# Kernel optimization log

Measured on AMD Instinct MI355X. Metric: run time of the kernel, lower is better.

## Reference

```python
import jax, jax.numpy as jnp
import numpy as np

N_USER = 500_000
N_GROUP = 100_000
N_EDGE = 5_000_000
DIM = 64
NORM_2 = -1.0  # exponent for back-pass degree norm (module default)
ALPHA = 0.0    # residual mix coefficient (module default)


def setup_inputs() -> dict:
    key = jax.random.key(0)
    k1, k2, k3, k4 = jax.random.split(key, 4)
    h_user = jax.random.normal(k1, (N_USER, DIM), dtype=jnp.float32)
    h_group = jax.random.normal(k2, (N_GROUP, DIM), dtype=jnp.float32)
    edge_src = jax.random.randint(k3, (N_EDGE,), 0, N_USER, dtype=jnp.int64)
    edge_dst = jax.random.randint(k4, (N_EDGE,), 0, N_GROUP, dtype=jnp.int64)
    return {"h_user": h_user, "h_group": h_group,
            "edge_src": edge_src, "edge_dst": edge_dst}


def reference(h_user, h_group, edge_src, edge_dst):
    # Forward pass: copy_src -> sum aggregate onto dst, normalize by in-degree^-1.
    ones = jnp.ones((edge_src.shape[0],), dtype=h_user.dtype)
    deg_dst = jax.ops.segment_sum(ones, edge_dst, num_segments=N_GROUP)
    deg_dst = jnp.maximum(deg_dst, 1.0)  # clamp(min=1)
    rst = jax.ops.segment_sum(h_user[edge_src], edge_dst, num_segments=N_GROUP)
    if ALPHA != 0.0:
        rst = rst + ALPHA * h_group
    rst = rst * (1.0 / deg_dst)[:, None]  # [N_GROUP, DIM]
    # Back pass: aggregate rst back onto src via reversed edges, normalize by deg^norm_2.
    deg_src = jax.ops.segment_sum(ones, edge_src, num_segments=N_USER)
    deg_src = jnp.maximum(deg_src, 1.0)
    bsrc = jax.ops.segment_sum(rst[edge_dst], edge_src, num_segments=N_USER)
    bsrc = bsrc * jnp.power(deg_src, NORM_2)[:, None]  # [N_USER, DIM]
    return bsrc, rst
```

## Files before the change

### kernel.cpp

```cpp
#include <hip/hip_runtime.h>

#define N_USER  500000
#define N_GROUP 100000
#define N_EDGE  5000000
#define DIM     64

#define SCAN_BLOCK 256
#define SCAN_ELEMS 4096
#define PER_THREAD (SCAN_ELEMS / SCAN_BLOCK)

#define KD_SHIFT 7
#define KS_SHIFT 9
#define C_DST ((N_GROUP + (1 << KD_SHIFT) - 1) >> KD_SHIFT)
#define C_SRC ((N_USER  + (1 << KS_SHIFT) - 1) >> KS_SHIFT)
#define TILE_A 16384
#define CVT_BLOCKS 1024
#define CAP_D 7680
#define CAP_S 6272

typedef unsigned int uint32;

__device__ inline unsigned short f2bf(float x) {
    uint32 b = __float_as_uint(x);
    uint32 r = (b + 0x7FFFu + ((b >> 16) & 1u)) >> 16;
    return (unsigned short)r;
}
__device__ inline float ldt(const float* t, size_t i) { return t[i]; }
__device__ inline float ldt(const unsigned short* t, size_t i) {
    return __uint_as_float((uint32)t[i] << 16);
}

__global__ void prep_kernel(const int* __restrict__ src,
                            const int* __restrict__ dst,
                            int* __restrict__ ccd,
                            int* __restrict__ ccs,
                            const float* __restrict__ hin,
                            unsigned short* __restrict__ h16,
                            int gridA) {
    __shared__ int hd[C_DST], hs[C_SRC];
    int tid = threadIdx.x;
    if ((int)blockIdx.x < gridA) {
        long base = (long)blockIdx.x * TILE_A;
        for (int k = tid; k < C_DST; k += blockDim.x) hd[k] = 0;
        for (int k = tid; k < C_SRC; k += blockDim.x) hs[k] = 0;
        __syncthreads();
        for (int i = tid; i < TILE_A; i += blockDim.x) {
            long e = base + i;
            if (e >= N_EDGE) break;
            atomicAdd(&hd[dst[e] >> KD_SHIFT], 1);
            atomicAdd(&hs[src[e] >> KS_SHIFT], 1);
        }
        __syncthreads();
        for (int k = tid; k < C_DST; k += blockDim.x) if (hd[k]) atomicAdd(&ccd[k], hd[k]);
        for (int k = tid; k < C_SRC; k += blockDim.x) if (hs[k]) atomicAdd(&ccs[k], hs[k]);
    } else if (h16) {
        long n4 = (long)N_USER * DIM / 4;
        long stride = (long)CVT_BLOCKS * blockDim.x;
        for (long i = (long)(blockIdx.x - gridA) * blockDim.x + tid; i < n4; i += stride) {
            const float4 v = ((const float4*)hin)[i];
            ushort4 o;
            o.x = f2bf(v.x); o.y = f2bf(v.y); o.z = f2bf(v.z); o.w = f2bf(v.w);
            ((ushort4*)h16)[i] = o;
        }
    }
}

#define SS_PT 16
__global__ void small_scan(const int* __restrict__ cnt,
                           int* __restrict__ coff,
                           int* __restrict__ curs,
                           int n,
                           int* __restrict__ tail) {
    __shared__ int tsum[256];
    int tid = threadIdx.x;
    int local[SS_PT];
    int sum = 0;
    int base = tid * SS_PT;
#pragma unroll
    for (int i = 0; i < SS_PT; ++i) {
        int idx = base + i;
        int v = (idx < n) ? cnt[idx] : 0;
        local[i] = sum;
        sum += v;
    }
    tsum[tid] = sum;
    __syncthreads();
    for (int o = 1; o < 256; o <<= 1) {
        int t = (tid >= o) ? tsum[tid - o] : 0;
        __syncthreads();
        tsum[tid] += t;
        __syncthreads();
    }
    int texc = tsum[tid] - sum;
    int total = tsum[255];
#pragma unroll
    for (int i = 0; i < SS_PT; ++i) {
        int idx = base + i;
        if (idx < n) {
            int v = texc + local[i];
            coff[idx] = v;
            curs[idx * 16] = v;
        }
    }
    if (tid == 0) {
        coff[n] = total;
        if (tail) *tail = total;
    }
}

__global__ void scan1_kernel(const int* __restrict__ cnt,
                             int* __restrict__ off,
                             int* __restrict__ partial,
                             int n) {
    __shared__ int sh[SCAN_BLOCK];
    int tid = threadIdx.x;
    int tbase = blockIdx.x * SCAN_ELEMS + tid * PER_THREAD;
    int local[PER_THREAD];
    int sum = 0;
#pragma unroll
    for (int i = 0; i < PER_THREAD; ++i) {
        int idx = tbase + i;
        int v = (idx < n) ? cnt[idx] : 0;
        local[i] = sum;
        sum += v;
    }
    sh[tid] = sum;
    __syncthreads();
    for (int o = 1; o < SCAN_BLOCK; o <<= 1) {
        int t = (tid >= o) ? sh[tid - o] : 0;
        __syncthreads();
        sh[tid] += t;
        __syncthreads();
    }
    int texc = sh[tid] - sum;
    int blockTotal = sh[SCAN_BLOCK - 1];
#pragma unroll
    for (int i = 0; i < PER_THREAD; ++i) {
        int idx = tbase + i;
        if (idx < n) off[idx] = local[i] + texc;
    }
    if (tid == 0) partial[blockIdx.x] = blockTotal;
}

__global__ void scan2_kernel(int* __restrict__ partial, int nb,
                             int* __restrict__ off_end) {
    __shared__ int sh[SCAN_BLOCK];
    int tid = threadIdx.x;
    int v = (tid < nb) ? partial[tid] : 0;
    sh[tid] = v;
    __syncthreads();
    for (int o = 1; o < SCAN_BLOCK; o <<= 1) {
        int t = (tid >= o) ? sh[tid - o] : 0;
        __syncthreads();
        sh[tid] += t;
        __syncthreads();
    }
    if (tid < nb) partial[tid] = sh[tid] - v;
    if (tid == 0) *off_end = sh[SCAN_BLOCK - 1];
}

__global__ void scan3_kernel(int* __restrict__ off,
                             const int* __restrict__ partial, int n) {
    int base = blockIdx.x * SCAN_ELEMS;
    int add = partial[blockIdx.x];
    for (int i = threadIdx.x; i < SCAN_ELEMS; i += blockDim.x) {
        int idx = base + i;
        if (idx < n) off[idx] += add;
    }
}

__global__ void passA(const int* __restrict__ src,
                      const int* __restrict__ dst,
                      int* __restrict__ curs_cd,
                      int* __restrict__ curs_cs,
                      uint32* __restrict__ coarse_dst,
                      uint32* __restrict__ coarse_src) {
    __shared__ int hd[C_DST], bd[C_DST], hs[C_SRC], bs[C_SRC];
    int tid = threadIdx.x;
    long base = (long)blockIdx.x * TILE_A;

    for (int c = tid; c < C_DST; c += blockDim.x) hd[c] = 0;
    for (int c = tid; c < C_SRC; c += blockDim.x) hs[c] = 0;
    __syncthreads();

    for (int i = tid; i < TILE_A; i += blockDim.x) {
        long e = base + i;
        if (e >= N_EDGE) break;
        int g = dst[e], u = src[e];
        atomicAdd(&hd[g >> KD_SHIFT], 1);
        atomicAdd(&hs[u >> KS_SHIFT], 1);
    }
    __syncthreads();

    for (int c = tid; c < C_DST; c += blockDim.x) {
        int n = hd[c];
        bd[c] = n ? atomicAdd(&curs_cd[c * 16], n) : 0;
        hd[c] = 0;
    }
    for (int c = tid; c < C_SRC; c += blockDim.x) {
        int n = hs[c];
        bs[c] = n ? atomicAdd(&curs_cs[c * 16], n) : 0;
        hs[c] = 0;
    }
    __syncthreads();

    for (int i = tid; i < TILE_A; i += blockDim.x) {
        long e = base + i;
        if (e >= N_EDGE) break;
        int g = dst[e], u = src[e];
        int cd = g >> KD_SHIFT;
        int pd = atomicAdd(&hd[cd], 1);
        coarse_dst[(size_t)bd[cd] + pd] =
            ((uint32)(g & ((1 << KD_SHIFT) - 1)) << 20) | (uint32)u;
        int cs = u >> KS_SHIFT;
        int ps = atomicAdd(&hs[cs], 1);
        coarse_src[(size_t)bs[cs] + ps] =
            ((uint32)(u & ((1 << KS_SHIFT) - 1)) << 20) | (uint32)g;
    }
}

template <int SHIFT, int CAP, int U, bool NT, typename T>
__global__ __launch_bounds__(512) void sortgather(
    const uint32* __restrict__ coarse,
    const int* __restrict__ coarse_off,
    const T* __restrict__ table,
    float* __restrict__ out,
    unsigned short* __restrict__ out16,
    int n) {
    const int NK = 1 << SHIFT;
    __shared__ int vals[CAP];
    __shared__ int hist[NK];
    __shared__ int cur[NK];
    int tid = threadIdx.x;
    int c = blockIdx.x;
    int lo_g = c << SHIFT;
    int beg = coarse_off[c], end = coarse_off[c + 1];
    int cnt = end - beg;
    int stg = min(cnt, CAP);

    for (int k = tid; k < NK; k += 512) hist[k] = 0;
    __syncthreads();

    for (int i = tid; i < stg; i += 512) {
        uint32 kv = coarse[beg + i];
        atomicAdd(&hist[kv >> 20], 1);
    }
    __syncthreads();

    for (int o = 1; o < NK; o <<= 1) {
        int t = (tid < NK && tid >= o) ? hist[tid - o] : 0;
        __syncthreads();
        if (tid < NK) hist[tid] += t;
        __syncthreads();
    }
    if (tid < NK) cur[tid] = (tid == 0) ? 0 : hist[tid - 1];
    __syncthreads();

    for (int i = tid; i < stg; i += 512) {
        uint32 kv = coarse[beg + i];
        int p = atomicAdd(&cur[kv >> 20], 1);
        vals[p] = (int)(kv & 0xFFFFFu);
    }
    __syncthreads();

    int wv = tid >> 6, lane = tid & 63;
    for (int r = wv; r < NK; r += 8) {
        int row = lo_g + r;
        if (row >= n) break;
        int lo = (r == 0) ? 0 : hist[r - 1];
        int hi = hist[r];
        float a[U];
#pragma unroll
        for (int j = 0; j < U; ++j) a[j] = 0.0f;
        int e = lo;
        for (; e + U <= hi; e += U) {
#pragma unroll
            for (int j = 0; j < U; ++j) {
                int s = vals[e + j];
                a[j] += ldt(table, (size_t)s * DIM + lane);
            }
        }
        for (; e < hi; ++e) {
            int s = vals[e];
            a[0] += ldt(table, (size_t)s * DIM + lane);
        }
        int deg = hi - lo;
        if (stg < cnt) {
            for (int i = beg + stg; i < end; ++i) {
                uint32 kv = coarse[i];
                if ((int)(kv >> 20) == r) {
                    a[0] += ldt(table, (size_t)(kv & 0xFFFFFu) * DIM + lane);
                    ++deg;
                }
            }
        }
        float acc = 0.0f;
#pragma unroll
        for (int j = 0; j < U; ++j) acc += a[j];
        float rv = acc / fmaxf((float)deg, 1.0f);
        size_t oidx = (size_t)row * DIM + lane;
        if (NT) __builtin_nontemporal_store(rv, &out[oidx]);
        else out[oidx] = rv;
        if (out16) out16[oidx] = f2bf(rv);
    }
}

__global__ void hist_kernel(const int* __restrict__ src,
                            const int* __restrict__ dst,
                            int* __restrict__ cnt_src,
                            int* __restrict__ cnt_dst) {
    int e = blockIdx.x * blockDim.x + threadIdx.x;
    if (e < N_EDGE) {
        atomicAdd(&cnt_src[src[e]], 1);
        atomicAdd(&cnt_dst[dst[e]], 1);
    }
}

__global__ void fill_both(const int* __restrict__ src,
                          const int* __restrict__ dst,
                          const int* __restrict__ off_src,
                          const int* __restrict__ off_dst,
                          int* __restrict__ cur_src,
                          int* __restrict__ cur_dst,
                          int* __restrict__ bucket_src,
                          int* __restrict__ bucket_dst) {
    int e = blockIdx.x * blockDim.x + threadIdx.x;
    if (e < N_EDGE) {
        int u = src[e];
        int g = dst[e];
        int p = atomicAdd(&cur_src[u], 1);
        bucket_src[off_src[u] + p] = g;
        int q = atomicAdd(&cur_dst[g], 1);
        bucket_dst[off_dst[g] + q] = u;
    }
}

__global__ void fill_one(const int* __restrict__ key,
                         const int* __restrict__ val,
                         const int* __restrict__ off,
                         int* __restrict__ cur,
                         int* __restrict__ bucket) {
    int e = blockIdx.x * blockDim.x + threadIdx.x;
    if (e < N_EDGE) {
        int k = key[e];
        int p = atomicAdd(&cur[k], 1);
        bucket[off[k] + p] = val[e];
    }
}

__global__ void cvt_bf16(const float* __restrict__ in,
                         unsigned short* __restrict__ out, long n4) {
    long i = (long)blockIdx.x * blockDim.x + threadIdx.x;
    if (i >= n4) return;
    const float4 v = ((const float4*)in)[i];
    ushort4 o;
    o.x = f2bf(v.x); o.y = f2bf(v.y); o.z = f2bf(v.z); o.w = f2bf(v.w);
    ((ushort4*)out)[i] = o;
}

template <int NROW, bool NT, int U, typename T>
__global__ void gather_kernel(const int* __restrict__ off,
                              const int* __restrict__ bucket,
                              const T* __restrict__ table,
                              float* __restrict__ out,
                              unsigned short* __restrict__ out16) {
    int wid = (blockIdx.x * blockDim.x + threadIdx.x) >> 6;
    int lane = threadIdx.x & 63;
    if (wid >= NROW) return;
    int beg = off[wid], end = off[wid + 1];

    float a[U];
#pragma unroll
    for (int j = 0; j < U; ++j) a[j] = 0.0f;

    for (int b = beg; b < end; b += 64) {
        int navail = min(64, end - b);
        int sv = bucket[b + (lane < navail ? lane : 0)];
        int k = 0;
        for (; k + U <= navail; k += U) {
#pragma unroll
            for (int j = 0; j < U; ++j) {
                int s = __shfl(sv, k + j);
                a[j] += ldt(table, (size_t)s * DIM + lane);
            }
        }
        if (k < navail) {
#pragma unroll
            for (int j = 0; j < U; ++j) {
                int kk = k + j;
                int s = __shfl(sv, kk < navail ? kk : navail - 1);
                float w = (kk < navail) ? 1.0f : 0.0f;
                a[j] += w * ldt(table, (size_t)s * DIM + lane);
            }
        }
    }
    float acc = 0.0f;
#pragma unroll
    for (int j = 0; j < U; ++j) acc += a[j];
    float inv = 1.0f / fmaxf((float)(end - beg), 1.0f);
    float r = acc * inv;
    if (NT) {
        __builtin_nontemporal_store(r, &out[(size_t)wid * DIM + lane]);
    } else {
        out[(size_t)wid * DIM + lane] = r;
    }
    if (out16) out16[(size_t)wid * DIM + lane] = f2bf(r);
}

__global__ void deg_kernel(const int* __restrict__ src,
                           const int* __restrict__ dst,
                           float* __restrict__ deg_src,
                           float* __restrict__ deg_dst) {
    int e = blockIdx.x * blockDim.x + threadIdx.x;
    if (e < N_EDGE) {
        unsafeAtomicAdd(&deg_src[src[e]], 1.0f);
        unsafeAtomicAdd(&deg_dst[dst[e]], 1.0f);
    }
}

__global__ void scatter_fwd(const int* __restrict__ src,
                            const int* __restrict__ dst,
                            const float* __restrict__ h_user,
                            float* __restrict__ rst) {
    long idx = (long)blockIdx.x * blockDim.x + threadIdx.x;
    if (idx >= (long)N_EDGE * DIM) return;
    int e = (int)(idx >> 6), d = (int)(idx & 63);
    unsafeAtomicAdd(&rst[(long)dst[e] * DIM + d], h_user[(long)src[e] * DIM + d]);
}

__global__ void norm_kernel(float* __restrict__ x,
                            const float* __restrict__ deg, long total) {
    long idx = (long)blockIdx.x * blockDim.x + threadIdx.x;
    if (idx >= total) return;
    float dg = fmaxf(deg[idx >> 6], 1.0f);
    x[idx] *= (1.0f / dg);
}

__global__ void scatter_bwd(const int* __restrict__ src,
                            const int* __restrict__ dst,
                            const float* __restrict__ rst,
                            float* __restrict__ bsrc) {
    long idx = (long)blockIdx.x * blockDim.x + threadIdx.x;
    if (idx >= (long)N_EDGE * DIM) return;
    int e = (int)(idx >> 6), d = (int)(idx & 63);
    unsafeAtomicAdd(&bsrc[(long)src[e] * DIM + d], rst[(long)dst[e] * DIM + d]);
}

extern "C" void kernel_launch(void* const* d_in, const int* in_sizes, int n_in,
                              void* d_out, int out_size, void* d_ws, size_t ws_size,
                              hipStream_t stream) {
    const float* h_user   = (const float*)d_in[0];
    const int*   edge_src = (const int*)d_in[2];
    const int*   edge_dst = (const int*)d_in[3];

    float* bsrc = (float*)d_out;
    float* rst  = bsrc + (size_t)N_USER * DIM;

    const int BLK = 256;
    const int grid_e = (N_EDGE + BLK - 1) / BLK;

    int* ws      = (int*)d_ws;
    int* cnt_dst = ws;
    int* off_dst = cnt_dst + N_GROUP;
    int* cnt_src = off_dst + N_GROUP + 1;
    int* off_src = cnt_src + N_USER;
    int* cur_dst = off_src + N_USER + 1;
    int* cur_src = cur_dst + N_GROUP;
    int* partial = cur_src + N_USER;
    int* bucket_dst = partial + 256;
    int* bucket_src = bucket_dst + N_EDGE;
    unsigned short* r16 = (unsigned short*)(bucket_src + N_EDGE);
    unsigned short* h16 = r16 + (size_t)N_GROUP * DIM;
    size_t tail = ((size_t)((char*)(h16 + (size_t)N_USER * DIM) - (char*)d_ws) + 7) & ~(size_t)7;
    int* curs_cd = (int*)((char*)d_ws + tail);
    int* curs_cs = curs_cd + C_DST * 16;
    int* ccnt_d  = curs_cs + C_SRC * 16;
    int* ccnt_s  = ccnt_d + C_DST;
    int* coff_d  = ccnt_s + C_SRC;
    int* coff_s  = coff_d + C_DST + 1;
    size_t tail2 = ((size_t)((char*)(coff_s + C_SRC + 1) - (char*)d_ws) + 7) & ~(size_t)7;
    uint32* coarse_dst = (uint32*)((char*)d_ws + tail2);
    uint32* coarse_src = coarse_dst + N_EDGE;

    size_t need_csr1 = (size_t)((bucket_dst + N_EDGE) - ws) * sizeof(int);
    size_t need_csr2 = (size_t)((bucket_src + N_EDGE) - ws) * sizeof(int);
    size_t need_r16  = need_csr2 + (size_t)N_GROUP * DIM * 2;
    size_t need_full = need_r16 + (size_t)N_USER * DIM * 2;
    size_t need_ms   = (size_t)((char*)(coarse_src + N_EDGE) - (char*)d_ws);

    int nb_dst = (N_GROUP + SCAN_ELEMS - 1) / SCAN_ELEMS;
    int nb_src = (N_USER + SCAN_ELEMS - 1) / SCAN_ELEMS;

    if (ws_size >= need_ms) {
        bool use_h16 = (ws_size >= need_full);
        bool use_r16 = (ws_size >= need_r16);

        hipMemsetAsync(ccnt_d, 0, (size_t)(C_DST + C_SRC) * sizeof(int), stream);

        int gridA = (N_EDGE + TILE_A - 1) / TILE_A;
        int gridP = gridA + (use_h16 ? CVT_BLOCKS : 0);
        prep_kernel<<<gridP, BLK, 0, stream>>>(edge_src, edge_dst, ccnt_d, ccnt_s,
                                               h_user, use_h16 ? h16 : nullptr, gridA);

        small_scan<<<1, 256, 0, stream>>>(ccnt_d, coff_d, curs_cd, C_DST, nullptr);
        small_scan<<<1, 256, 0, stream>>>(ccnt_s, coff_s, curs_cs, C_SRC, nullptr);

        passA<<<gridA, BLK, 0, stream>>>(edge_src, edge_dst,
                                         curs_cd, curs_cs, coarse_dst, coarse_src);

        unsigned short* r16p = use_r16 ? r16 : (unsigned short*)nullptr;
        if (use_h16) {
            sortgather<KD_SHIFT, CAP_D, 8, false, unsigned short>
                <<<C_DST, 512, 0, stream>>>(coarse_dst, coff_d, h16, rst, r16p, N_GROUP);
        } else {
            sortgather<KD_SHIFT, CAP_D, 8, false, float>
                <<<C_DST, 512, 0, stream>>>(coarse_dst, coff_d, h_user, rst, r16p, N_GROUP);
        }
        if (use_r16) {
            sortgather<KS_SHIFT, CAP_S, 4, true, unsigned short>
                <<<C_SRC, 512, 0, stream>>>(coarse_src, coff_s, r16, bsrc, nullptr, N_USER);
        } else {
            sortgather<KS_SHIFT, CAP_S, 4, true, float>
                <<<C_SRC, 512, 0, stream>>>(coarse_src, coff_s, rst, bsrc, nullptr, N_USER);
        }
        return;
    }

    if (ws_size >= need_csr2) {
        bool use_h16 = (ws_size >= need_full);
        bool use_r16 = (ws_size >= need_r16);

        hipMemsetAsync(d_ws, 0, (size_t)(partial - ws) * sizeof(int), stream);

        if (use_h16) {
            long n4 = (long)N_USER * DIM / 4;
            cvt_bf16<<<(int)((n4 + BLK - 1) / BLK), BLK, 0, stream>>>(h_user, h16, n4);
        }

        hist_kernel<<<grid_e, BLK, 0, stream>>>(edge_src, edge_dst, cnt_src, cnt_dst);

        scan1_kernel<<<nb_dst, SCAN_BLOCK, 0, stream>>>(cnt_dst, off_dst, partial, N_GROUP);
        scan2_kernel<<<1, SCAN_BLOCK, 0, stream>>>(partial, nb_dst, off_dst + N_GROUP);
        scan3_kernel<<<nb_dst, SCAN_BLOCK, 0, stream>>>(off_dst, partial, N_GROUP);

        scan1_kernel<<<nb_src, SCAN_BLOCK, 0, stream>>>(cnt_src, off_src, partial, N_USER);
        scan2_kernel<<<1, SCAN_BLOCK, 0, stream>>>(partial, nb_src, off_src + N_USER);
        scan3_kernel<<<nb_src, SCAN_BLOCK, 0, stream>>>(off_src, partial, N_USER);

        fill_both<<<grid_e, BLK, 0, stream>>>(
            edge_src, edge_dst, off_src, off_dst,
            cur_src, cur_dst, bucket_src, bucket_dst);

        unsigned short* r16p = use_r16 ? r16 : (unsigned short*)nullptr;
        if (use_h16) {
            gather_kernel<N_GROUP, false, 8, unsigned short>
                <<<(N_GROUP * 64 + BLK - 1) / BLK, BLK, 0, stream>>>(
                    off_dst, bucket_dst, h16, rst, r16p);
        } else {
            gather_kernel<N_GROUP, false, 8, float>
                <<<(N_GROUP * 64 + BLK - 1) / BLK, BLK, 0, stream>>>(
                    off_dst, bucket_dst, h_user, rst, r16p);
        }
        if (use_r16) {
            gather_kernel<N_USER, true, 4, unsigned short>
                <<<(int)(((size_t)N_USER * 64 + BLK - 1) / BLK), BLK, 0, stream>>>(
                    off_src, bucket_src, r16, bsrc, nullptr);
        } else {
            gather_kernel<N_USER, true, 4, float>
                <<<(int)(((size_t)N_USER * 64 + BLK - 1) / BLK), BLK, 0, stream>>>(
                    off_src, bucket_src, rst, bsrc, nullptr);
        }
        return;
    }

    if (ws_size >= need_csr1) {
        hipMemsetAsync(d_ws, 0, (size_t)(partial - ws) * sizeof(int), stream);
        hist_kernel<<<grid_e, BLK, 0, stream>>>(edge_src, edge_dst, cnt_src, cnt_dst);

        scan1_kernel<<<nb_dst, SCAN_BLOCK, 0, stream>>>(cnt_dst, off_dst, partial, N_GROUP);
        scan2_kernel<<<1, SCAN_BLOCK, 0, stream>>>(partial, nb_dst, off_dst + N_GROUP);
        scan3_kernel<<<nb_dst, SCAN_BLOCK, 0, stream>>>(off_dst, partial, N_GROUP);

        scan1_kernel<<<nb_src, SCAN_BLOCK, 0, stream>>>(cnt_src, off_src, partial, N_USER);
        scan2_kernel<<<1, SCAN_BLOCK, 0, stream>>>(partial, nb_src, off_src + N_USER);
        scan3_kernel<<<nb_src, SCAN_BLOCK, 0, stream>>>(off_src, partial, N_USER);

        fill_one<<<grid_e, BLK, 0, stream>>>(edge_dst, edge_src, off_dst, cur_dst, bucket_dst);
        gather_kernel<N_GROUP, false, 8, float>
            <<<(N_GROUP * 64 + BLK - 1) / BLK, BLK, 0, stream>>>(
                off_dst, bucket_dst, h_user, rst, nullptr);

        fill_one<<<grid_e, BLK, 0, stream>>>(edge_src, edge_dst, off_src, cur_src, bucket_dst);
        gather_kernel<N_USER, true, 4, float>
            <<<(int)(((size_t)N_USER * 64 + BLK - 1) / BLK), BLK, 0, stream>>>(
                off_src, bucket_dst, rst, bsrc, nullptr);
        return;
    }

    float* deg_dst = (float*)d_ws;
    float* deg_src = deg_dst + N_GROUP;
    hipMemsetAsync(d_out, 0, (size_t)(N_USER + N_GROUP) * DIM * sizeof(float), stream);
    hipMemsetAsync(d_ws, 0, (size_t)(N_USER + N_GROUP) * sizeof(float), stream);

    deg_kernel<<<grid_e, BLK, 0, stream>>>(edge_src, edge_dst, deg_src, deg_dst);

    long total_ed = (long)N_EDGE * DIM;
    int grid_ed = (int)((total_ed + BLK - 1) / BLK);
    scatter_fwd<<<grid_ed, BLK, 0, stream>>>(edge_src, edge_dst, h_user, rst);
    long total_g = (long)N_GROUP * DIM;
    norm_kernel<<<(int)((total_g + BLK - 1) / BLK), BLK, 0, stream>>>(rst, deg_dst, total_g);
    scatter_bwd<<<grid_ed, BLK, 0, stream>>>(edge_src, edge_dst, rst, bsrc);
    long total_u = (long)N_USER * DIM;
    norm_kernel<<<(int)((total_u + BLK - 1) / BLK), BLK, 0, stream>>>(bsrc, deg_src, total_u);
}
```

Before: 597.9 us.

## Replace atomic bucket cursors with scanned per-block count matrix; split rst into halves

Each prep block now writes its per-bucket counts into a bucket-major count matrix, and a full three-stage scan over that matrix gives every block fixed write offsets. This removes the global atomics on bucket cursors and the second histogram pass in passA, and it also makes the scatter deterministic. The bf16 copy of rst is stored as two 32-column halves, and a new backward kernel gathers each half in its own pass, so every gathered row is 64 bytes. This is meant to improve cache hit rates on the random gathers. In exchange it adds six scan launches over the large matrices and reads the edge lists twice in the backward kernel.

```diff
diff --git a/kernel.cpp b/kernel.cpp
--- a/kernel.cpp
+++ b/kernel.cpp
@@ -14,9 +14,12 @@
 #define C_DST ((N_GROUP + (1 << KD_SHIFT) - 1) >> KD_SHIFT)
 #define C_SRC ((N_USER  + (1 << KS_SHIFT) - 1) >> KS_SHIFT)
 #define TILE_A 16384
+#define GRID_A ((N_EDGE + TILE_A - 1) / TILE_A)
 #define CVT_BLOCKS 1024
 #define CAP_D 7680
 #define CAP_S 6272
+#define MD_N (C_DST * GRID_A)
+#define MS_N (C_SRC * GRID_A)
 
 typedef unsigned int uint32;
 
@@ -32,15 +35,15 @@
 
 __global__ void prep_kernel(const int* __restrict__ src,
                             const int* __restrict__ dst,
-                            int* __restrict__ ccd,
-                            int* __restrict__ ccs,
+                            int* __restrict__ mat_d,
+                            int* __restrict__ mat_s,
                             const float* __restrict__ hin,
-                            unsigned short* __restrict__ h16,
-                            int gridA) {
+                            unsigned short* __restrict__ h16) {
     __shared__ int hd[C_DST], hs[C_SRC];
     int tid = threadIdx.x;
-    if ((int)blockIdx.x < gridA) {
-        long base = (long)blockIdx.x * TILE_A;
+    int b = blockIdx.x;
+    if (b < GRID_A) {
+        long base = (long)b * TILE_A;
         for (int k = tid; k < C_DST; k += blockDim.x) hd[k] = 0;
         for (int k = tid; k < C_SRC; k += blockDim.x) hs[k] = 0;
         __syncthreads();
@@ -51,60 +54,17 @@
             atomicAdd(&hs[src[e] >> KS_SHIFT], 1);
         }
         __syncthreads();
-        for (int k = tid; k < C_DST; k += blockDim.x) if (hd[k]) atomicAdd(&ccd[k], hd[k]);
-        for (int k = tid; k < C_SRC; k += blockDim.x) if (hs[k]) atomicAdd(&ccs[k], hs[k]);
+        for (int k = tid; k < C_DST; k += blockDim.x) mat_d[(size_t)k * GRID_A + b] = hd[k];
+        for (int k = tid; k < C_SRC; k += blockDim.x) mat_s[(size_t)k * GRID_A + b] = hs[k];
     } else if (h16) {
         long n4 = (long)N_USER * DIM / 4;
         long stride = (long)CVT_BLOCKS * blockDim.x;
-        for (long i = (long)(blockIdx.x - gridA) * blockDim.x + tid; i < n4; i += stride) {
+        for (long i = (long)(b - GRID_A) * blockDim.x + tid; i < n4; i += stride) {
             const float4 v = ((const float4*)hin)[i];
             ushort4 o;
             o.x = f2bf(v.x); o.y = f2bf(v.y); o.z = f2bf(v.z); o.w = f2bf(v.w);
             ((ushort4*)h16)[i] = o;
         }
-    }
-}
-
-#define SS_PT 16
-__global__ void small_scan(const int* __restrict__ cnt,
-                           int* __restrict__ coff,
-                           int* __restrict__ curs,
-                           int n,
-                           int* __restrict__ tail) {
-    __shared__ int tsum[256];
-    int tid = threadIdx.x;
-    int local[SS_PT];
-    int sum = 0;
-    int base = tid * SS_PT;
-#pragma unroll
-    for (int i = 0; i < SS_PT; ++i) {
-        int idx = base + i;
-        int v = (idx < n) ? cnt[idx] : 0;
-        local[i] = sum;
-        sum += v;
-    }
-    tsum[tid] = sum;
-    __syncthreads();
-    for (int o = 1; o < 256; o <<= 1) {
-        int t = (tid >= o) ? tsum[tid - o] : 0;
-        __syncthreads();
-        tsum[tid] += t;
-        __syncthreads();
-    }
-    int texc = tsum[tid] - sum;
-    int total = tsum[255];
-#pragma unroll
-    for (int i = 0; i < SS_PT; ++i) {
-        int idx = base + i;
-        if (idx < n) {
-            int v = texc + local[i];
-            coff[idx] = v;
-            curs[idx * 16] = v;
-        }
-    }
-    if (tid == 0) {
-        coff[n] = total;
-        if (tail) *tail = total;
     }
 }
 
@@ -171,37 +131,17 @@
 
 __global__ void passA(const int* __restrict__ src,
                       const int* __restrict__ dst,
-                      int* __restrict__ curs_cd,
-                      int* __restrict__ curs_cs,
+                      const int* __restrict__ mat_d,
+                      const int* __restrict__ mat_s,
                       uint32* __restrict__ coarse_dst,
                       uint32* __restrict__ coarse_src) {
-    __shared__ int hd[C_DST], bd[C_DST], hs[C_SRC], bs[C_SRC];
+    __shared__ int bd[C_DST], bs[C_SRC];
     int tid = threadIdx.x;
-    long base = (long)blockIdx.x * TILE_A;
-
-    for (int c = tid; c < C_DST; c += blockDim.x) hd[c] = 0;
-    for (int c = tid; c < C_SRC; c += blockDim.x) hs[c] = 0;
-    __syncthreads();
-
-    for (int i = tid; i < TILE_A; i += blockDim.x) {
-        long e = base + i;
-        if (e >= N_EDGE) break;
-        int g = dst[e], u = src[e];
-        atomicAdd(&hd[g >> KD_SHIFT], 1);
-        atomicAdd(&hs[u >> KS_SHIFT], 1);
-    }
-    __syncthreads();
-
-    for (int c = tid; c < C_DST; c += blockDim.x) {
-        int n = hd[c];
-        bd[c] = n ? atomicAdd(&curs_cd[c * 16], n) : 0;
-        hd[c] = 0;
-    }
-    for (int c = tid; c < C_SRC; c += blockDim.x) {
-        int n = hs[c];
-        bs[c] = n ? atomicAdd(&curs_cs[c * 16], n) : 0;
-        hs[c] = 0;
-    }
+    int b = blockIdx.x;
+    long base = (long)b * TILE_A;
+
+    for (int c = tid; c < C_DST; c += blockDim.x) bd[c] = mat_d[(size_t)c * GRID_A + b];
+    for (int c = tid; c < C_SRC; c += blockDim.x) bs[c] = mat_s[(size_t)c * GRID_A + b];
     __syncthreads();
 
     for (int i = tid; i < TILE_A; i += blockDim.x) {
@@ -209,23 +149,22 @@
         if (e >= N_EDGE) break;
         int g = dst[e], u = src[e];
         int cd = g >> KD_SHIFT;
-        int pd = atomicAdd(&hd[cd], 1);
-        coarse_dst[(size_t)bd[cd] + pd] =
-            ((uint32)(g & ((1 << KD_SHIFT) - 1)) << 20) | (uint32)u;
+        int pd = atomicAdd(&bd[cd], 1);
+        coarse_dst[pd] = ((uint32)(g & ((1 << KD_SHIFT) - 1)) << 20) | (uint32)u;
         int cs = u >> KS_SHIFT;
-        int ps = atomicAdd(&hs[cs], 1);
-        coarse_src[(size_t)bs[cs] + ps] =
-            ((uint32)(u & ((1 << KS_SHIFT) - 1)) << 20) | (uint32)g;
+        int ps = atomicAdd(&bs[cs], 1);
+        coarse_src[ps] = ((uint32)(u & ((1 << KS_SHIFT) - 1)) << 20) | (uint32)g;
     }
 }
 
 template <int SHIFT, int CAP, int U, bool NT, typename T>
 __global__ __launch_bounds__(512) void sortgather(
     const uint32* __restrict__ coarse,
-    const int* __restrict__ coarse_off,
+    const int* __restrict__ mat,
     const T* __restrict__ table,
     float* __restrict__ out,
-    unsigned short* __restrict__ out16,
+    unsigned short* __restrict__ p0,
+    unsigned short* __restrict__ p1,
     int n) {
     const int NK = 1 << SHIFT;
     __shared__ int vals[CAP];
@@ -234,7 +173,8 @@
     int tid = threadIdx.x;
     int c = blockIdx.x;
     int lo_g = c << SHIFT;
-    int beg = coarse_off[c], end = coarse_off[c + 1];
+    int beg = mat[(size_t)c * GRID_A];
+    int end = mat[(size_t)(c + 1) * GRID_A];
     int cnt = end - beg;
     int stg = min(cnt, CAP);
 
@@ -242,8 +182,7 @@
     __syncthreads();
 
     for (int i = tid; i < stg; i += 512) {
-        uint32 kv = coarse[beg + i];
-        atomicAdd(&hist[kv >> 20], 1);
+        atomicAdd(&hist[coarse[beg + i] >> 20], 1);
     }
     __syncthreads();
 
@@ -301,7 +240,95 @@
         size_t oidx = (size_t)row * DIM + lane;
         if (NT) __builtin_nontemporal_store(rv, &out[oidx]);
         else out[oidx] = rv;
-        if (out16) out16[oidx] = f2bf(rv);
+        if (p0) {
+            unsigned short bv = f2bf(rv);
+            if (lane < 32) p0[(size_t)row * 32 + lane] = bv;
+            else           p1[(size_t)row * 32 + (lane - 32)] = bv;
+        }
+    }
+}
+
+template <int SHIFT, int CAP>
+__global__ __launch_bounds__(512) void sortgather_bwd(
+    const uint32* __restrict__ coarse,
+    const int* __restrict__ mat,
+    const unsigned short* __restrict__ p0,
+    const unsigned short* __restrict__ p1,
+    float* __restrict__ out,
+    int n) {
+    const int NK = 1 << SHIFT;
+    __shared__ int vals[CAP];
+    __shared__ int hist[NK];
+    __shared__ int cur[NK];
+    int tid = threadIdx.x;
+    int c = blockIdx.x;
+    int lo_g = c << SHIFT;
+    int beg = mat[(size_t)c * GRID_A];
+    int end = mat[(size_t)(c + 1) * GRID_A];
+    int cnt = end - beg;
+    int stg = min(cnt, CAP);
+
+    for (int k = tid; k < NK; k += 512) hist[k] = 0;
+    __syncthreads();
+    for (int i = tid; i < stg; i += 512) {
+        atomicAdd(&hist[coarse[beg + i] >> 20], 1);
+    }
+    __syncthreads();
+    for (int o = 1; o < NK; o <<= 1) {
+        int t = (tid < NK && tid >= o) ? hist[tid - o] : 0;
+        __syncthreads();
+        if (tid < NK) hist[tid] += t;
+        __syncthreads();
+    }
+    if (tid < NK) cur[tid] = (tid == 0) ? 0 : hist[tid - 1];
+    __syncthreads();
+    for (int i = tid; i < stg; i += 512) {
+        uint32 kv = coarse[beg + i];
+        int p = atomicAdd(&cur[kv >> 20], 1);
+        vals[p] = (int)(kv & 0xFFFFFu);
+    }
+    __syncthreads();
+
+    int wv = tid >> 6, lane = tid & 63;
+    int sub = lane >> 5, d = lane & 31;
+    for (int h = 0; h < 2; ++h) {
+        const unsigned short* pl = h ? p1 : p0;
+        for (int r = wv; r < NK; r += 8) {
+            int row = lo_g + r;
+            if (row >= n) break;
+            int lo = (r == 0) ? 0 : hist[r - 1];
+            int hi = hist[r];
+            int deg = hi - lo;
+            float a = 0.0f, b2 = 0.0f;
+            int e = lo;
+            for (; e + 4 <= hi; e += 4) {
+                int s0 = vals[e + sub];
+                int s1 = vals[e + 2 + sub];
+                a  += ldt(pl, (size_t)s0 * 32 + d);
+                b2 += ldt(pl, (size_t)s1 * 32 + d);
+            }
+            for (; e < hi; e += 2) {
+                int ee = e + sub;
+                float w = (ee < hi) ? 1.0f : 0.0f;
+                int s = vals[ee < hi ? ee : hi - 1];
+                a += w * ldt(pl, (size_t)s * 32 + d);
+            }
+            if (stg < cnt) {
+                for (int i = beg + stg; i < end; ++i) {
+                    uint32 kv = coarse[i];
+                    if ((int)(kv >> 20) == r) {
+                        float w = (sub == 0) ? 1.0f : 0.0f;
+                        a += w * ldt(pl, (size_t)(kv & 0xFFFFFu) * 32 + d);
+                        ++deg;
+                    }
+                }
+            }
+            float s = a + b2;
+            s += __shfl_xor(s, 32);
+            float rv = s / fmaxf((float)deg, 1.0f);
+            if (sub == 0)
+                __builtin_nontemporal_store(rv, &out[(size_t)row * DIM + h * 32 + d]);
+        }
     }
 }
 
@@ -471,14 +498,12 @@
     int* bucket_src = bucket_dst + N_EDGE;
     unsigned short* r16 = (unsigned short*)(bucket_src + N_EDGE);
     unsigned short* h16 = r16 + (size_t)N_GROUP * DIM;
+    unsigned short* rp0 = r16;
+    unsigned short* rp1 = r16 + (size_t)N_GROUP * 32;
     size_t tail = ((size_t)((char*)(h16 + (size_t)N_USER * DIM) - (char*)d_ws) + 7) & ~(size_t)7;
-    int* curs_cd = (int*)((char*)d_ws + tail);
-    int* curs_cs = curs_cd + C_DST * 16;
-    int* ccnt_d  = curs_cs + C_SRC * 16;
-    int* ccnt_s  = ccnt_d + C_DST;
-    int* coff_d  = ccnt_s + C_SRC;
-    int* coff_s  = coff_d + C_DST + 1;
-    size_t tail2 = ((size_t)((char*)(coff_s + C_SRC + 1) - (char*)d_ws) + 7) & ~(size_t)7;
+    int* mat_d = (int*)((char*)d_ws + tail);
+    int* mat_s = mat_d + MD_N + 1;
+    size_t tail2 = ((size_t)((char*)(mat_s + MS_N + 1) - (char*)d_ws) + 7) & ~(size_t)7;
     uint32* coarse_dst = (uint32*)((char*)d_ws + tail2);
     uint32* coarse_src = coarse_dst + N_EDGE;
 
@@ -495,33 +520,40 @@
         bool use_h16 = (ws_size >= need_full);
         bool use_r16 = (ws_size >= need_r16);
 
-        hipMemsetAsync(ccnt_d, 0, (size_t)(C_DST + C_SRC) * sizeof(int), stream);
-
-        int gridA = (N_EDGE + TILE_A - 1) / TILE_A;
-        int gridP = gridA + (use_h16 ? CVT_BLOCKS : 0);
-        prep_kernel<<<gridP, BLK, 0, stream>>>(edge_src, edge_dst, ccnt_d, ccnt_s,
-                                               h_user, use_h16 ? h16 : nullptr, gridA);
-
-        small_scan<<<1, 256, 0, stream>>>(ccnt_d, coff_d, curs_cd, C_DST, nullptr);
-        small_scan<<<1, 256, 0, stream>>>(ccnt_s, coff_s, curs_cs, C_SRC, nullptr);
-
-        passA<<<gridA, BLK, 0, stream>>>(edge_src, edge_dst,
-                                         curs_cd, curs_cs, coarse_dst, coarse_src);
-
-        unsigned short* r16p = use_r16 ? r16 : (unsigned short*)nullptr;
+        int gridP = GRID_A + (use_h16 ? CVT_BLOCKS : 0);
+        prep_kernel<<<gridP, BLK, 0, stream>>>(edge_src, edge_dst, mat_d, mat_s,
+                                               h_user, use_h16 ? h16 : nullptr);
+
+        int nb_md = (MD_N + SCAN_ELEMS - 1) / SCAN_ELEMS;
+        int nb_ms = (MS_N + SCAN_ELEMS - 1) / SCAN_ELEMS;
+        scan1_kernel<<<nb_md, SCAN_BLOCK, 0, stream>>>(mat_d, mat_d, partial, MD_N);
+        scan2_kernel<<<1, SCAN_BLOCK, 0, stream>>>(partial, nb_md, mat_d + MD_N);
+        scan3_kernel<<<nb_md, SCAN_BLOCK, 0, stream>>>(mat_d, partial, MD_N);
+        scan1_kernel<<<nb_ms, SCAN_BLOCK, 0, stream>>>(mat_s, mat_s, partial, MS_N);
+        scan2_kernel<<<1, SCAN_BLOCK, 0, stream>>>(partial, nb_ms, mat_s + MS_N);
+        scan3_kernel<<<nb_ms, SCAN_BLOCK, 0, stream>>>(mat_s, partial, MS_N);
+
+        passA<<<GRID_A, BLK, 0, stream>>>(edge_src, edge_dst, mat_d, mat_s,
+                                          coarse_dst, coarse_src);
+
         if (use_h16) {
             sortgather<KD_SHIFT, CAP_D, 8, false, unsigned short>
-                <<<C_DST, 512, 0, stream>>>(coarse_dst, coff_d, h16, rst, r16p, N_GROUP);
+                <<<C_DST, 512, 0, stream>>>(coarse_dst, mat_d, h16, rst,
+                                            use_r16 ? rp0 : nullptr,
+                                            use_r16 ? rp1 : nullptr, N_GROUP);
         } else {
             sortgather<KD_SHIFT, CAP_D, 8, false, float>
-                <<<C_DST, 512, 0, stream>>>(coarse_dst, coff_d, h_user, rst, r16p, N_GROUP);
+                <<<C_DST, 512, 0, stream>>>(coarse_dst, mat_d, h_user, rst,
+                                            use_r16 ? rp0 : nullptr,
+                                            use_r16 ? rp1 : nullptr, N_GROUP);
         }
         if (use_r16) {
-            sortgather<KS_SHIFT, CAP_S, 4, true, unsigned short>
-                <<<C_SRC, 512, 0, stream>>>(coarse_src, coff_s, r16, bsrc, nullptr, N_USER);
+            sortgather_bwd<KS_SHIFT, CAP_S>
+                <<<C_SRC, 512, 0, stream>>>(coarse_src, mat_s, rp0, rp1, bsrc, N_USER);
         } else {
             sortgather<KS_SHIFT, CAP_S, 4, true, float>
-                <<<C_SRC, 512, 0, stream>>>(coarse_src, coff_s, rst, bsrc, nullptr, N_USER);
+                <<<C_SRC, 512, 0, stream>>>(coarse_src, mat_s, rst, bsrc,
+                                            nullptr, nullptr, N_USER);
         }
         return;
     }
```

Result: slower. 634.6 us (+6.1%).
